# Kernel tuning notes

Measured on AMD Instinct MI355X. Metric: run time of the kernel, lower is better.

Reference implementation:

```python
import jax, jax.numpy as jnp
import numpy as np

B, S, D = 2, 2048, 2048
H, H_KV, HD = 8, 1, 256   # attention heads, kv heads, head_dim
N_REP = H // H_KV


def setup_inputs() -> dict:
    key = jax.random.key(0)
    ks = jax.random.split(key, 8)
    std = 1.0 / np.sqrt(D)
    return {
        "hidden_states": jax.random.normal(ks[0], (B, S, D), dtype=jnp.float32),
        "attention_mask": jnp.zeros((B, 1, S, S), dtype=jnp.float32),
        "cos": jax.random.uniform(ks[1], (B, S, HD), dtype=jnp.float32),
        "sin": jax.random.uniform(ks[2], (B, S, HD), dtype=jnp.float32),
        "Wq": jax.random.normal(ks[3], (D, H * HD), dtype=jnp.float32) * std,
        "Wk": jax.random.normal(ks[4], (D, H_KV * HD), dtype=jnp.float32) * std,
        "Wv": jax.random.normal(ks[5], (D, H_KV * HD), dtype=jnp.float32) * std,
        "Wo": jax.random.normal(ks[6], (H * HD, D), dtype=jnp.float32) * std,
    }


def _rotate_half(x):
    x1, x2 = jnp.split(x, 2, axis=-1)
    return jnp.concatenate((-x2, x1), axis=-1)


def reference(hidden_states, attention_mask, cos, sin, Wq, Wk, Wv, Wo):
    b, s, _ = hidden_states.shape
    # projections -> [b, heads, s, hd]
    q = (hidden_states @ Wq).reshape(b, s, H, HD).transpose(0, 2, 1, 3)
    k = (hidden_states @ Wk).reshape(b, s, H_KV, HD).transpose(0, 2, 1, 3)
    v = (hidden_states @ Wv).reshape(b, s, H_KV, HD).transpose(0, 2, 1, 3)
    # RoPE (unsqueeze_dim=1)
    c = cos[:, None, :, :]
    sn = sin[:, None, :, :]
    q = q * c + _rotate_half(q) * sn
    k = k * c + _rotate_half(k) * sn
    # GQA: repeat kv heads
    k = jnp.repeat(k, N_REP, axis=1)
    v = jnp.repeat(v, N_REP, axis=1)
    # attention
    scores = jnp.einsum("bhqd,bhkd->bhqk", q, k) / jnp.sqrt(jnp.float32(HD))
    scores = scores + attention_mask[:, :, :, :k.shape[2]]
    attn_weights = jax.nn.softmax(scores.astype(jnp.float32), axis=-1).astype(q.dtype)
    # dropout p=0.0 -> identity
    out = jnp.einsum("bhqk,bhkd->bhqd", attn_weights, v)
    out = out.transpose(0, 2, 1, 3).reshape(b, s, H * HD)
    out = out @ Wo
    return out, attn_weights
```

## Files before the change

kernel.cpp:

```cpp
#include <hip/hip_runtime.h>
#include <hip/hip_bf16.h>

typedef float f32x4 __attribute__((ext_vector_type(4)));
typedef short short8 __attribute__((ext_vector_type(8)));
typedef unsigned int uint2v __attribute__((ext_vector_type(2)));

#define DI __device__ __forceinline__

DI unsigned short f2bf(float f) {
  unsigned int u = __float_as_uint(f);
  u += 0x7fffu + ((u >> 16) & 1u);
  return (unsigned short)(u >> 16);
}

DI float bf2f(unsigned short u) {
  union { unsigned int i; float f; } x;
  x.i = ((unsigned int)u) << 16;
  return x.f;
}

DI unsigned int packbf(float a, float b) {
  return (unsigned int)f2bf(a) | ((unsigned int)f2bf(b) << 16);
}

DI void gload16(const unsigned short* g, unsigned short* l) {
  __builtin_amdgcn_global_load_lds((const __attribute__((address_space(1))) void*)g,
                                   (__attribute__((address_space(3))) void*)l, 16, 0, 0);
}

__global__ void cvt_bf16_kernel(const float* __restrict__ src,
                                unsigned short* __restrict__ dst, long n) {
  long i = ((long)blockIdx.x * blockDim.x + threadIdx.x) * 8;
  if (i >= n) return;
  f32x4 a = __builtin_nontemporal_load((const f32x4*)(src + i));
  f32x4 b = __builtin_nontemporal_load((const f32x4*)(src + i + 4));
  short8 v;
  v[0] = f2bf(a[0]); v[1] = f2bf(a[1]); v[2] = f2bf(a[2]); v[3] = f2bf(a[3]);
  v[4] = f2bf(b[0]); v[5] = f2bf(b[1]); v[6] = f2bf(b[2]); v[7] = f2bf(b[3]);
  *(short8*)(dst + i) = v;
}

__global__ void transpose_cvt_kernel(const float* __restrict__ src,
                                     unsigned short* __restrict__ dst,
                                     int ldsrc, int lddst, long sBatch, long dBatch) {
  __shared__ float tile[32][33];
  const float* s = src + (long)blockIdx.z * sBatch;
  unsigned short* d = dst + (long)blockIdx.z * dBatch;
  int c0 = blockIdx.x * 32, r0 = blockIdx.y * 32;
  int tx = threadIdx.x, ty = threadIdx.y;
#pragma unroll
  for (int k = 0; k < 4; k++)
    tile[ty + 8 * k][tx] =
        __builtin_nontemporal_load(s + (long)(r0 + ty + 8 * k) * ldsrc + c0 + tx);
  __syncthreads();
#pragma unroll
  for (int k = 0; k < 4; k++)
    d[(long)(c0 + ty + 8 * k) * lddst + r0 + tx] = f2bf(tile[tx][ty + 8 * k]);
}

__global__ void transpose_v_kernel(const float* __restrict__ qkv,
                                   unsigned short* __restrict__ VtC) {
  __shared__ float tile[32][33];
  int b = blockIdx.z;
  int d0 = blockIdx.x * 32, s0 = blockIdx.y * 32;
  int tx = threadIdx.x, ty = threadIdx.y;
  const float* s = qkv + (long)b * 2048 * 2560 + 2304;
#pragma unroll
  for (int k = 0; k < 4; k++)
    tile[ty + 8 * k][tx] = s[(long)(s0 + ty + 8 * k) * 2560 + d0 + tx];
  __syncthreads();
  unsigned short* d = VtC + (long)b * 524288 + (long)(s0 >> 5) * 8192;
#pragma unroll
  for (int k = 0; k < 4; k++) {
    int dd = d0 + ty + 8 * k;
    d[dd * 32 + (tx ^ (((dd >> 1) & 3) << 3))] = f2bf(tile[tx][ty + 8 * k]);
  }
}

__global__ void rope_kernel(const float* __restrict__ qkv, const float* __restrict__ cs,
                            const float* __restrict__ sn, unsigned short* __restrict__ Qb,
                            unsigned short* __restrict__ Ksw) {
  int bs = blockIdx.x;
  int d = threadIdx.x;
  long ci = (long)bs * 256 + d;
  float cv = cs[ci], sv = sn[ci];
  int b = bs >> 11, s2 = bs & 2047;
  const float* row = qkv + (long)bs * 2560;
  int off = (d < 128) ? 128 : -128;
  float sgn = (d < 128) ? -1.f : 1.f;
#pragma unroll
  for (int hp = 0; hp < 9; hp++) {
    float x = row[hp * 256 + d];
    float o = sgn * row[hp * 256 + d + off];
    unsigned short v = f2bf(x * cv + o * sv);
    if (hp < 8) {
      Qb[((long)(b * 8 + hp) * 2048 + s2) * 256 + d] = v;
    } else {
      Ksw[(long)bs * 256 + (d ^ ((bs & 7) << 3))] = v;
    }
  }
}

template <bool AF32, bool CBF16, bool CNT>
__launch_bounds__(256)
__global__ void gemm_bt_kernel(const void* __restrict__ Av,
                               const unsigned short* __restrict__ Btg,
                               void* __restrict__ Cv,
                               int K, int lda, int ldb, int ldc,
                               int zShift, long aBatch, long bBatch, long cBatch, long cHead) {
  __shared__ unsigned short Asm_[128 * 32];
  __shared__ unsigned short Bsm_[128 * 32];
  int z = blockIdx.z;
  int zb = z >> zShift, zh = z - (zb << zShift);
  const unsigned short* Bt = Btg + (long)zb * bBatch;
  const unsigned short* A16 = (const unsigned short*)Av + (long)z * aBatch;
  const float* A32 = (const float*)Av + (long)z * aBatch;
  int nwg = gridDim.x * gridDim.y;
  int bid = blockIdx.y * gridDim.x + blockIdx.x;
  int qq = nwg >> 3;
  int swz = (bid & 7) * qq + (bid >> 3);
  int m0 = (swz / gridDim.x) * 128, n0 = (swz % gridDim.x) * 128;
  int tid = threadIdx.x, w = tid >> 6, lane = tid & 63, c = lane & 15, t = lane >> 4;
  int wm = w >> 1, wn = w & 1;
  f32x4 zero4 = {0.f, 0.f, 0.f, 0.f};
  f32x4 acc[4][4];
#pragma unroll
  for (int i = 0; i < 4; i++)
#pragma unroll
    for (int j = 0; j < 4; j++) acc[i][j] = zero4;

  for (int kt = 0; kt < K; kt += 32) {
    if constexpr (!AF32) {
#pragma unroll
      for (int jj = 0; jj < 2; jj++) {
        int slot = (w * 2 + jj) * 64 + lane;
        int r = slot >> 2, g = slot & 3;
        int gs = g ^ ((r >> 1) & 3);
        gload16(A16 + (long)(m0 + r) * lda + kt + gs * 8, Asm_ + slot * 8);
      }
    } else {
#pragma unroll
      for (int jj = 0; jj < 2; jj++) {
        int slot = jj * 256 + tid;
        int r = slot >> 2, g = slot & 3;
        int gs = g ^ ((r >> 1) & 3);
        const float* p = A32 + (long)(m0 + r) * lda + kt + gs * 8;
        float4 x = *(const float4*)p;
        float4 y = *(const float4*)(p + 4);
        short8 v;
        v[0] = f2bf(x.x); v[1] = f2bf(x.y); v[2] = f2bf(x.z); v[3] = f2bf(x.w);
        v[4] = f2bf(y.x); v[5] = f2bf(y.y); v[6] = f2bf(y.z); v[7] = f2bf(y.w);
        *(short8*)(Asm_ + slot * 8) = v;
      }
    }
#pragma unroll
    for (int jj = 0; jj < 2; jj++) {
      int slot = (w * 2 + jj) * 64 + lane;
      int r = slot >> 2, g = slot & 3;
      int gs = g ^ ((r >> 1) & 3);
      gload16(Bt + (long)(n0 + r) * ldb + kt + gs * 8, Bsm_ + slot * 8);
    }
    __syncthreads();
    short8 af[4], bfg[4];
#pragma unroll
    for (int mi = 0; mi < 4; mi++) {
      int r = wm * 64 + mi * 16 + c;
      af[mi] = *(const short8*)(Asm_ + r * 32 + ((t ^ ((r >> 1) & 3)) * 8));
    }
#pragma unroll
    for (int ni = 0; ni < 4; ni++) {
      int r = wn * 64 + ni * 16 + c;
      bfg[ni] = *(const short8*)(Bsm_ + r * 32 + ((t ^ ((r >> 1) & 3)) * 8));
    }
#pragma unroll
    for (int mi = 0; mi < 4; mi++)
#pragma unroll
      for (int ni = 0; ni < 4; ni++)
        acc[mi][ni] = __builtin_amdgcn_mfma_f32_16x16x32_bf16(af[mi], bfg[ni], acc[mi][ni], 0, 0, 0);
    __syncthreads();
  }
  long cOff = (long)zb * cBatch + zh * cHead;
#pragma unroll
  for (int mi = 0; mi < 4; mi++) {
#pragma unroll
    for (int j = 0; j < 4; j++) {
      int row = m0 + wm * 64 + mi * 16 + t * 4 + j;
#pragma unroll
      for (int ni = 0; ni < 4; ni++) {
        int col = n0 + wn * 64 + ni * 16 + c;
        float v = acc[mi][ni][j];
        long idx = cOff + (long)row * ldc + col;
        if constexpr (CBF16) {
          ((unsigned short*)Cv)[idx] = f2bf(v);
        } else if constexpr (CNT) {
          __builtin_nontemporal_store(v, (float*)Cv + idx);
        } else {
          ((float*)Cv)[idx] = v;
        }
      }
    }
  }
}

#define KC 32
__launch_bounds__(512, 4)
__global__ void attn_fused_kernel(const unsigned short* __restrict__ Qb,
                                  const unsigned short* __restrict__ Ksw,
                                  const unsigned short* __restrict__ VtC,
                                  const float* __restrict__ mask,
                                  float* __restrict__ attnW,
                                  unsigned short* __restrict__ attnO) {
  __shared__ unsigned short Ksm[2][KC * 256];
  __shared__ unsigned short Vsm[2][256 * KC];
  __shared__ unsigned short Pt[2][4][16 * 32];
  __shared__ float red[8][16];
  const int id = blockIdx.x;
  const int sw = (id & 7) * 64 + (id >> 3);
  const int qblk = sw & 31, bh = sw >> 5;
  const int b = bh >> 3;
  const int tid = threadIdx.x, w = tid >> 6, lane = tid & 63;
  const int c = lane & 15, t = lane >> 4;
  const int s = w & 3, h = w >> 2;
  const int q0 = qblk * 64 + s * 16;
  const int kh = 16 * h;
  const float scale = 0.0625f;

  short8 qf[8];
  {
    const unsigned short* Qrow = Qb + ((long)bh * 2048 + q0 + c) * 256 + t * 8;
#pragma unroll
    for (int ks = 0; ks < 8; ks++) qf[ks] = *(const short8*)(Qrow + ks * 32);
  }

  const unsigned short* Kg = Ksw + (long)b * 524288;
  const unsigned short* Vg = VtC + (long)b * 524288;
  const float* mrow = mask + (long)b * 4194304 + (long)(q0 + c) * 2048 + kh + t * 4;

  float lp = 0.f;

#pragma unroll
  for (int i = 0; i < 2; i++) {
    int slot = i * 512 + tid;
    gload16(Kg + slot * 8, Ksm[0] + slot * 8);
  }
  f32x4 mv = *(const f32x4*)(mrow);
  for (int kc = 0; kc < 64; kc++) {
    int cur = kc & 1;
    asm volatile("s_barrier" ::: "memory");
    f32x4 mvn;
    if (kc < 63) {
      const unsigned short* src = Kg + (long)(kc + 1) * 8192;
#pragma unroll
      for (int i = 0; i < 2; i++) {
        int slot = i * 512 + tid;
        gload16(src + slot * 8, Ksm[cur ^ 1] + slot * 8);
      }
      mvn = *(const f32x4*)(mrow + (kc + 1) * 32);
      asm volatile("s_waitcnt vmcnt(3)" ::: "memory");
    } else {
      asm volatile("s_waitcnt vmcnt(0)" ::: "memory");
    }
    __builtin_amdgcn_sched_barrier(0);
    f32x4 a0 = {0.f, 0.f, 0.f, 0.f};
    __builtin_amdgcn_s_setprio(1);
#pragma unroll
    for (int ks = 0; ks < 8; ks++) {
      int g0 = ((ks * 4 + t) ^ (c & 7)) * 8;
      short8 kf = *(const short8*)(Ksm[cur] + (kh + c) * 256 + g0);
      a0 = __builtin_amdgcn_mfma_f32_16x16x32_bf16(kf, qf[ks], a0, 0, 0, 0);
    }
    __builtin_amdgcn_s_setprio(0);
#pragma unroll
    for (int j = 0; j < 4; j++) lp += __expf(a0[j] * scale + mv[j]);
    mv = mvn;
  }
  lp += __shfl_xor(lp, 16);
  lp += __shfl_xor(lp, 32);
  if (t == 0) red[w][c] = lp;
  __syncthreads();
  float rinv = 1.0f / (red[s][c] + red[4 + s][c]);

  float* awB = attnW + (long)bh * 4194304 + (long)(qblk * 64) * 2048;
  const int psw = ((c >> 1) & 3) << 3;
  const int srow = tid >> 3, sqk = tid & 7;
  const int ss2 = srow >> 4, sc2 = srow & 15;
  const int spsw = ((sc2 >> 1) & 3) << 3;
  const unsigned short* pRd = &Pt[0][ss2][0] + sc2 * 32 + ((sqk * 4) ^ spsw);
  const int ptStride = 4 * 16 * 32;
  float* awRow = awB + (long)srow * 2048 + sqk * 4;
  f32x4 accO[8];
#pragma unroll
  for (int i = 0; i < 8; i++) accO[i] = (f32x4){0.f, 0.f, 0.f, 0.f};

#pragma unroll
  for (int i = 0; i < 2; i++) {
    int slot = i * 512 + tid;
    gload16(Kg + slot * 8, Ksm[0] + slot * 8);
  }
  mv = *(const f32x4*)(mrow);
  for (int kc = 0; kc < 64; kc++) {
    int cur = kc & 1;
    asm volatile("s_barrier" ::: "memory");
    f32x4 mvn;
    if (kc < 63) {
      const unsigned short* ksrc = Kg + (long)(kc + 1) * 8192;
      const unsigned short* vsrc = Vg + (long)kc * 8192;
#pragma unroll
      for (int i = 0; i < 2; i++) {
        int slot = i * 512 + tid;
        gload16(ksrc + slot * 8, Ksm[cur ^ 1] + slot * 8);
        gload16(vsrc + slot * 8, Vsm[cur] + slot * 8);
      }
      mvn = *(const f32x4*)(mrow + (kc + 1) * 32);
      asm volatile("s_waitcnt vmcnt(5)" ::: "memory");
    } else {
      const unsigned short* vsrc = Vg + (long)kc * 8192;
#pragma unroll
      for (int i = 0; i < 2; i++) {
        int slot = i * 512 + tid;
        gload16(vsrc + slot * 8, Vsm[cur] + slot * 8);
      }
      asm volatile("s_waitcnt vmcnt(2)" ::: "memory");
    }
    __builtin_amdgcn_sched_barrier(0);
    f32x4 a0 = {0.f, 0.f, 0.f, 0.f};
    __builtin_amdgcn_s_setprio(1);
#pragma unroll
    for (int ks = 0; ks < 8; ks++) {
      int g0 = ((ks * 4 + t) ^ (c & 7)) * 8;
      short8 kf = *(const short8*)(Ksm[cur] + (kh + c) * 256 + g0);
      a0 = __builtin_amdgcn_mfma_f32_16x16x32_bf16(kf, qf[ks], a0, 0, 0, 0);
    }
    __builtin_amdgcn_s_setprio(0);
    f32x4 p;
#pragma unroll
    for (int j = 0; j < 4; j++) p[j] = __expf(a0[j] * scale + mv[j]) * rinv;
    mv = mvn;
    uint2v pw;
    pw[0] = packbf(p[0], p[1]); pw[1] = packbf(p[2], p[3]);
    *(uint2v*)(&Pt[cur][s][0] + c * 32 + ((kh + t * 4) ^ psw)) = pw;
    if (kc >= 1) {
      uint2v pu = *(const uint2v*)(pRd + (cur ^ 1) * ptStride);
      f32x4 aw;
      aw[0] = bf2f((unsigned short)(pu[0] & 0xffff));
      aw[1] = bf2f((unsigned short)(pu[0] >> 16));
      aw[2] = bf2f((unsigned short)(pu[1] & 0xffff));
      aw[3] = bf2f((unsigned short)(pu[1] >> 16));
      __builtin_nontemporal_store(aw, (f32x4*)(awRow + (kc - 1) * 32));
      short8 pa = *(const short8*)(&Pt[cur ^ 1][s][0] + c * 32 + ((t * 8) ^ psw));
      __builtin_amdgcn_s_setprio(1);
#pragma unroll
      for (int di = 0; di < 8; di++) {
        int d = (8 * h + di) * 16 + c;
        short8 vf = *(const short8*)(Vsm[cur ^ 1] + d * 32 + ((t * 8) ^ psw));
        accO[di] = __builtin_amdgcn_mfma_f32_16x16x32_bf16(pa, vf, accO[di], 0, 0, 0);
      }
      __builtin_amdgcn_s_setprio(0);
    }
    asm volatile("s_waitcnt lgkmcnt(0)" ::: "memory");
  }
  asm volatile("s_waitcnt vmcnt(0)" ::: "memory");
  __builtin_amdgcn_s_barrier();
  __builtin_amdgcn_sched_barrier(0);
  {
    uint2v pu = *(const uint2v*)(pRd + 1 * ptStride);
    f32x4 aw;
    aw[0] = bf2f((unsigned short)(pu[0] & 0xffff));
    aw[1] = bf2f((unsigned short)(pu[0] >> 16));
    aw[2] = bf2f((unsigned short)(pu[1] & 0xffff));
    aw[3] = bf2f((unsigned short)(pu[1] >> 16));
    __builtin_nontemporal_store(aw, (f32x4*)(awRow + 63 * 32));
    short8 pa = *(const short8*)(&Pt[1][s][0] + c * 32 + ((t * 8) ^ psw));
#pragma unroll
    for (int di = 0; di < 8; di++) {
      int d = (8 * h + di) * 16 + c;
      short8 vf = *(const short8*)(Vsm[1] + d * 32 + ((t * 8) ^ psw));
      accO[di] = __builtin_amdgcn_mfma_f32_16x16x32_bf16(pa, vf, accO[di], 0, 0, 0);
    }
  }
  long obase = ((long)b * 2048 + q0 + t * 4) * 2048 + (bh & 7) * 256 + h * 128 + c;
#pragma unroll
  for (int di = 0; di < 8; di++)
#pragma unroll
    for (int j = 0; j < 4; j++)
      __builtin_nontemporal_store(f2bf(accO[di][j]),
                                  attnO + obase + (long)j * 2048 + di * 16);
}

extern "C" void kernel_launch(void* const* d_in, const int* in_sizes, int n_in,
                              void* d_out, int out_size, void* d_ws, size_t ws_size,
                              hipStream_t stream) {
  const float* hidden = (const float*)d_in[0];
  const float* mask = (const float*)d_in[1];
  const float* cosb = (const float*)d_in[2];
  const float* sinb = (const float*)d_in[3];
  const float* Wq = (const float*)d_in[4];
  const float* Wk = (const float*)d_in[5];
  const float* Wv = (const float*)d_in[6];
  const float* Wo = (const float*)d_in[7];
  float* out = (float*)d_out;
  float* attnW = out + 8388608;

  char* ws = (char*)d_ws;
  unsigned short* hidB  = (unsigned short*)(ws + 0);
  unsigned short* WqkvT = (unsigned short*)(ws + 16777216);
  unsigned short* WoT   = (unsigned short*)(ws + 27262976);
  float*          qkv   = (float*)(ws + 35651584);
  unsigned short* Qb    = (unsigned short*)(ws + 77594624);
  unsigned short* Ksw   = (unsigned short*)(ws + 94371840);
  unsigned short* VtC   = (unsigned short*)(ws + 96468992);
  unsigned short* attnO = (unsigned short*)(ws + 98566144);

  cvt_bf16_kernel<<<4096, 256, 0, stream>>>(hidden, hidB, 8388608L);
  transpose_cvt_kernel<<<dim3(64, 64, 1), dim3(32, 8), 0, stream>>>(Wq, WqkvT, 2048, 2048, 0, 0);
  transpose_cvt_kernel<<<dim3(8, 64, 1), dim3(32, 8), 0, stream>>>(Wk, WqkvT + (long)2048 * 2048, 256, 2048, 0, 0);
  transpose_cvt_kernel<<<dim3(8, 64, 1), dim3(32, 8), 0, stream>>>(Wv, WqkvT + (long)2304 * 2048, 256, 2048, 0, 0);
  transpose_cvt_kernel<<<dim3(64, 64, 1), dim3(32, 8), 0, stream>>>(Wo, WoT, 2048, 2048, 0, 0);
  gemm_bt_kernel<false, false, false><<<dim3(20, 32, 1), 256, 0, stream>>>(
      hidB, WqkvT, qkv, 2048, 2048, 2048, 2560, 0, 0, 0, 0, 0);
  rope_kernel<<<4096, 256, 0, stream>>>(qkv, cosb, sinb, Qb, Ksw);
  transpose_v_kernel<<<dim3(8, 64, 2), dim3(32, 8), 0, stream>>>(qkv, VtC);
  attn_fused_kernel<<<512, 512, 0, stream>>>(Qb, Ksw, VtC, mask, attnW, attnO);
  gemm_bt_kernel<false, false, true><<<dim3(16, 32, 1), 256, 0, stream>>>(
      attnO, WoT, out, 2048, 2048, 2048, 2048, 0, 0, 0, 0, 0);
}
```

Measured before the change: 348.7 us.

## Halve attention block to four waves, each computing two 16-row query tiles

The fused attention kernel now runs 256 threads per block instead of 512. Each wave processes two 16-row query sub-tiles against each K/V fragment it loads from shared memory, so every LDS fragment read feeds two MFMAs. The change is meant to cut LDS read traffic and barrier cost per unit of work. In exchange, register pressure roughly doubles (two Q fragment sets, 16 output accumulators), the launch bounds drop to 2 blocks per CU, and each thread issues more global loads per chunk.

```diff
diff --git a/kernel.cpp b/kernel.cpp
--- a/kernel.cpp
+++ b/kernel.cpp
@@ -203,7 +203,7 @@
 }
 
 #define KC 32
-__launch_bounds__(512, 4)
+__launch_bounds__(256, 2)
 __global__ void attn_fused_kernel(const unsigned short* __restrict__ Qb,
                                   const unsigned short* __restrict__ Ksw,
                                   const unsigned short* __restrict__ VtC,
@@ -212,179 +212,220 @@
                                   unsigned short* __restrict__ attnO) {
   __shared__ unsigned short Ksm[2][KC * 256];
   __shared__ unsigned short Vsm[2][256 * KC];
-  __shared__ unsigned short Pt[2][4][16 * 32];
-  __shared__ float red[8][16];
+  __shared__ unsigned short Pt[2][2][2][16 * 32];
+  __shared__ float red[4][32];
   const int id = blockIdx.x;
   const int sw = (id & 7) * 64 + (id >> 3);
   const int qblk = sw & 31, bh = sw >> 5;
   const int b = bh >> 3;
   const int tid = threadIdx.x, w = tid >> 6, lane = tid & 63;
   const int c = lane & 15, t = lane >> 4;
-  const int s = w & 3, h = w >> 2;
-  const int q0 = qblk * 64 + s * 16;
+  const int g = w & 1, h = w >> 1;
+  const int qa = qblk * 64 + g * 32;
   const int kh = 16 * h;
   const float scale = 0.0625f;
 
-  short8 qf[8];
+  short8 qfa[8], qfb[8];
   {
-    const unsigned short* Qrow = Qb + ((long)bh * 2048 + q0 + c) * 256 + t * 8;
-#pragma unroll
-    for (int ks = 0; ks < 8; ks++) qf[ks] = *(const short8*)(Qrow + ks * 32);
+    const unsigned short* Qra = Qb + ((long)bh * 2048 + qa + c) * 256 + t * 8;
+    const unsigned short* Qrb = Qra + 16 * 256;
+#pragma unroll
+    for (int ks = 0; ks < 8; ks++) {
+      qfa[ks] = *(const short8*)(Qra + ks * 32);
+      qfb[ks] = *(const short8*)(Qrb + ks * 32);
+    }
   }
 
   const unsigned short* Kg = Ksw + (long)b * 524288;
   const unsigned short* Vg = VtC + (long)b * 524288;
-  const float* mrow = mask + (long)b * 4194304 + (long)(q0 + c) * 2048 + kh + t * 4;
-
-  float lp = 0.f;
-
-#pragma unroll
-  for (int i = 0; i < 2; i++) {
-    int slot = i * 512 + tid;
+  const float* mra = mask + (long)b * 4194304 + (long)(qa + c) * 2048 + kh + t * 4;
+  const float* mrb = mra + 16 * 2048;
+
+  float lp0 = 0.f, lp1 = 0.f;
+
+#pragma unroll
+  for (int i = 0; i < 4; i++) {
+    int slot = i * 256 + tid;
     gload16(Kg + slot * 8, Ksm[0] + slot * 8);
   }
-  f32x4 mv = *(const f32x4*)(mrow);
+  f32x4 mva = *(const f32x4*)(mra);
+  f32x4 mvb = *(const f32x4*)(mrb);
   for (int kc = 0; kc < 64; kc++) {
     int cur = kc & 1;
     asm volatile("s_barrier" ::: "memory");
-    f32x4 mvn;
+    f32x4 mna, mnb;
     if (kc < 63) {
       const unsigned short* src = Kg + (long)(kc + 1) * 8192;
 #pragma unroll
-      for (int i = 0; i < 2; i++) {
-        int slot = i * 512 + tid;
+      for (int i = 0; i < 4; i++) {
+        int slot = i * 256 + tid;
         gload16(src + slot * 8, Ksm[cur ^ 1] + slot * 8);
       }
-      mvn = *(const f32x4*)(mrow + (kc + 1) * 32);
-      asm volatile("s_waitcnt vmcnt(3)" ::: "memory");
+      mna = *(const f32x4*)(mra + (kc + 1) * 32);
+      mnb = *(const f32x4*)(mrb + (kc + 1) * 32);
+      asm volatile("s_waitcnt vmcnt(6)" ::: "memory");
     } else {
       asm volatile("s_waitcnt vmcnt(0)" ::: "memory");
     }
     __builtin_amdgcn_sched_barrier(0);
-    f32x4 a0 = {0.f, 0.f, 0.f, 0.f};
+    f32x4 a0 = {0.f, 0.f, 0.f, 0.f}, a1 = a0;
     __builtin_amdgcn_s_setprio(1);
 #pragma unroll
     for (int ks = 0; ks < 8; ks++) {
       int g0 = ((ks * 4 + t) ^ (c & 7)) * 8;
       short8 kf = *(const short8*)(Ksm[cur] + (kh + c) * 256 + g0);
-      a0 = __builtin_amdgcn_mfma_f32_16x16x32_bf16(kf, qf[ks], a0, 0, 0, 0);
+      a0 = __builtin_amdgcn_mfma_f32_16x16x32_bf16(kf, qfa[ks], a0, 0, 0, 0);
+      a1 = __builtin_amdgcn_mfma_f32_16x16x32_bf16(kf, qfb[ks], a1, 0, 0, 0);
     }
     __builtin_amdgcn_s_setprio(0);
 #pragma unroll
-    for (int j = 0; j < 4; j++) lp += __expf(a0[j] * scale + mv[j]);
-    mv = mvn;
-  }
-  lp += __shfl_xor(lp, 16);
-  lp += __shfl_xor(lp, 32);
-  if (t == 0) red[w][c] = lp;
+    for (int j = 0; j < 4; j++) {
+      lp0 += __expf(a0[j] * scale + mva[j]);
+      lp1 += __expf(a1[j] * scale + mvb[j]);
+    }
+    mva = mna; mvb = mnb;
+  }
+  lp0 += __shfl_xor(lp0, 16); lp0 += __shfl_xor(lp0, 32);
+  lp1 += __shfl_xor(lp1, 16); lp1 += __shfl_xor(lp1, 32);
+  if (t == 0) { red[w][c] = lp0; red[w][16 + c] = lp1; }
   __syncthreads();
-  float rinv = 1.0f / (red[s][c] + red[4 + s][c]);
-
+  float ri0 = 1.0f / (red[g][c] + red[g + 2][c]);
+  float ri1 = 1.0f / (red[g][16 + c] + red[g + 2][16 + c]);
+
+  const int psw = ((c >> 1) & 3) << 3;
   float* awB = attnW + (long)bh * 4194304 + (long)(qblk * 64) * 2048;
-  const int psw = ((c >> 1) & 3) << 3;
-  const int srow = tid >> 3, sqk = tid & 7;
-  const int ss2 = srow >> 4, sc2 = srow & 15;
-  const int spsw = ((sc2 >> 1) & 3) << 3;
-  const unsigned short* pRd = &Pt[0][ss2][0] + sc2 * 32 + ((sqk * 4) ^ spsw);
-  const int ptStride = 4 * 16 * 32;
-  float* awRow = awB + (long)srow * 2048 + sqk * 4;
-  f32x4 accO[8];
-#pragma unroll
-  for (int i = 0; i < 8; i++) accO[i] = (f32x4){0.f, 0.f, 0.f, 0.f};
-
-#pragma unroll
-  for (int i = 0; i < 2; i++) {
-    int slot = i * 512 + tid;
+  f32x4 accO[2][8];
+#pragma unroll
+  for (int i = 0; i < 2; i++)
+#pragma unroll
+    for (int j = 0; j < 8; j++) accO[i][j] = (f32x4){0.f, 0.f, 0.f, 0.f};
+
+#pragma unroll
+  for (int i = 0; i < 4; i++) {
+    int slot = i * 256 + tid;
     gload16(Kg + slot * 8, Ksm[0] + slot * 8);
   }
-  mv = *(const f32x4*)(mrow);
+  mva = *(const f32x4*)(mra);
+  mvb = *(const f32x4*)(mrb);
   for (int kc = 0; kc < 64; kc++) {
     int cur = kc & 1;
     asm volatile("s_barrier" ::: "memory");
-    f32x4 mvn;
+    f32x4 mna, mnb;
     if (kc < 63) {
       const unsigned short* ksrc = Kg + (long)(kc + 1) * 8192;
       const unsigned short* vsrc = Vg + (long)kc * 8192;
 #pragma unroll
-      for (int i = 0; i < 2; i++) {
-        int slot = i * 512 + tid;
+      for (int i = 0; i < 4; i++) {
+        int slot = i * 256 + tid;
         gload16(ksrc + slot * 8, Ksm[cur ^ 1] + slot * 8);
         gload16(vsrc + slot * 8, Vsm[cur] + slot * 8);
       }
-      mvn = *(const f32x4*)(mrow + (kc + 1) * 32);
-      asm volatile("s_waitcnt vmcnt(5)" ::: "memory");
+      mna = *(const f32x4*)(mra + (kc + 1) * 32);
+      mnb = *(const f32x4*)(mrb + (kc + 1) * 32);
+      asm volatile("s_waitcnt vmcnt(10)" ::: "memory");
     } else {
       const unsigned short* vsrc = Vg + (long)kc * 8192;
 #pragma unroll
-      for (int i = 0; i < 2; i++) {
-        int slot = i * 512 + tid;
+      for (int i = 0; i < 4; i++) {
+        int slot = i * 256 + tid;
         gload16(vsrc + slot * 8, Vsm[cur] + slot * 8);
       }
-      asm volatile("s_waitcnt vmcnt(2)" ::: "memory");
+      asm volatile("s_waitcnt vmcnt(4)" ::: "memory");
     }
     __builtin_amdgcn_sched_barrier(0);
-    f32x4 a0 = {0.f, 0.f, 0.f, 0.f};
+    f32x4 a0 = {0.f, 0.f, 0.f, 0.f}, a1 = a0;
     __builtin_amdgcn_s_setprio(1);
 #pragma unroll
     for (int ks = 0; ks < 8; ks++) {
       int g0 = ((ks * 4 + t) ^ (c & 7)) * 8;
       short8 kf = *(const short8*)(Ksm[cur] + (kh + c) * 256 + g0);
-      a0 = __builtin_amdgcn_mfma_f32_16x16x32_bf16(kf, qf[ks], a0, 0, 0, 0);
+      a0 = __builtin_amdgcn_mfma_f32_16x16x32_bf16(kf, qfa[ks], a0, 0, 0, 0);
+      a1 = __builtin_amdgcn_mfma_f32_16x16x32_bf16(kf, qfb[ks], a1, 0, 0, 0);
     }
     __builtin_amdgcn_s_setprio(0);
-    f32x4 p;
-#pragma unroll
-    for (int j = 0; j < 4; j++) p[j] = __expf(a0[j] * scale + mv[j]) * rinv;
-    mv = mvn;
-    uint2v pw;
-    pw[0] = packbf(p[0], p[1]); pw[1] = packbf(p[2], p[3]);
-    *(uint2v*)(&Pt[cur][s][0] + c * 32 + ((kh + t * 4) ^ psw)) = pw;
+    f32x4 p0, p1;
+#pragma unroll
+    for (int j = 0; j < 4; j++) {
+      p0[j] = __expf(a0[j] * scale + mva[j]) * ri0;
+      p1[j] = __expf(a1[j] * scale + mvb[j]) * ri1;
+    }
+    mva = mna; mvb = mnb;
+    uint2v pw0, pw1;
+    pw0[0] = packbf(p0[0], p0[1]); pw0[1] = packbf(p0[2], p0[3]);
+    pw1[0] = packbf(p1[0], p1[1]); pw1[1] = packbf(p1[2], p1[3]);
+    *(uint2v*)(&Pt[cur][g][0][0] + c * 32 + ((kh + t * 4) ^ psw)) = pw0;
+    *(uint2v*)(&Pt[cur][g][1][0] + c * 32 + ((kh + t * 4) ^ psw)) = pw1;
     if (kc >= 1) {
-      uint2v pu = *(const uint2v*)(pRd + (cur ^ 1) * ptStride);
+#pragma unroll
+      for (int li = 0; li < 2; li++) {
+        int slot2 = li * 256 + tid;
+        int srow = slot2 >> 3, sqk = slot2 & 7;
+        int sg = srow >> 5, ssub = (srow >> 4) & 1, sc2 = srow & 15;
+        int spsw2 = ((sc2 >> 1) & 3) << 3;
+        uint2v pu = *(const uint2v*)(&Pt[cur ^ 1][sg][ssub][0] + sc2 * 32 +
+                                     ((sqk * 4) ^ spsw2));
+        f32x4 aw;
+        aw[0] = bf2f((unsigned short)(pu[0] & 0xffff));
+        aw[1] = bf2f((unsigned short)(pu[0] >> 16));
+        aw[2] = bf2f((unsigned short)(pu[1] & 0xffff));
+        aw[3] = bf2f((unsigned short)(pu[1] >> 16));
+        __builtin_nontemporal_store(
+            aw, (f32x4*)(awB + (long)srow * 2048 + (kc - 1) * 32 + sqk * 4));
+      }
+      short8 pa0 = *(const short8*)(&Pt[cur ^ 1][g][0][0] + c * 32 + ((t * 8) ^ psw));
+      short8 pa1 = *(const short8*)(&Pt[cur ^ 1][g][1][0] + c * 32 + ((t * 8) ^ psw));
+      __builtin_amdgcn_s_setprio(1);
+#pragma unroll
+      for (int di = 0; di < 8; di++) {
+        int d = (8 * h + di) * 16 + c;
+        short8 vf = *(const short8*)(Vsm[cur ^ 1] + d * 32 + ((t * 8) ^ psw));
+        accO[0][di] = __builtin_amdgcn_mfma_f32_16x16x32_bf16(pa0, vf, accO[0][di], 0, 0, 0);
+        accO[1][di] = __builtin_amdgcn_mfma_f32_16x16x32_bf16(pa1, vf, accO[1][di], 0, 0, 0);
+      }
+      __builtin_amdgcn_s_setprio(0);
+    }
+    asm volatile("s_waitcnt lgkmcnt(0)" ::: "memory");
+  }
+  asm volatile("s_waitcnt vmcnt(0)" ::: "memory");
+  __builtin_amdgcn_s_barrier();
+  __builtin_amdgcn_sched_barrier(0);
+  {
+#pragma unroll
+    for (int li = 0; li < 2; li++) {
+      int slot2 = li * 256 + tid;
+      int srow = slot2 >> 3, sqk = slot2 & 7;
+      int sg = srow >> 5, ssub = (srow >> 4) & 1, sc2 = srow & 15;
+      int spsw2 = ((sc2 >> 1) & 3) << 3;
+      uint2v pu = *(const uint2v*)(&Pt[1][sg][ssub][0] + sc2 * 32 + ((sqk * 4) ^ spsw2));
       f32x4 aw;
       aw[0] = bf2f((unsigned short)(pu[0] & 0xffff));
       aw[1] = bf2f((unsigned short)(pu[0] >> 16));
       aw[2] = bf2f((unsigned short)(pu[1] & 0xffff));
       aw[3] = bf2f((unsigned short)(pu[1] >> 16));
-      __builtin_nontemporal_store(aw, (f32x4*)(awRow + (kc - 1) * 32));
-      short8 pa = *(const short8*)(&Pt[cur ^ 1][s][0] + c * 32 + ((t * 8) ^ psw));
-      __builtin_amdgcn_s_setprio(1);
-#pragma unroll
-      for (int di = 0; di < 8; di++) {
-        int d = (8 * h + di) * 16 + c;
-        short8 vf = *(const short8*)(Vsm[cur ^ 1] + d * 32 + ((t * 8) ^ psw));
-        accO[di] = __builtin_amdgcn_mfma_f32_16x16x32_bf16(pa, vf, accO[di], 0, 0, 0);
-      }
-      __builtin_amdgcn_s_setprio(0);
-    }
-    asm volatile("s_waitcnt lgkmcnt(0)" ::: "memory");
-  }
-  asm volatile("s_waitcnt vmcnt(0)" ::: "memory");
-  __builtin_amdgcn_s_barrier();
-  __builtin_amdgcn_sched_barrier(0);
-  {
-    uint2v pu = *(const uint2v*)(pRd + 1 * ptStride);
-    f32x4 aw;
-    aw[0] = bf2f((unsigned short)(pu[0] & 0xffff));
-    aw[1] = bf2f((unsigned short)(pu[0] >> 16));
-    aw[2] = bf2f((unsigned short)(pu[1] & 0xffff));
-    aw[3] = bf2f((unsigned short)(pu[1] >> 16));
-    __builtin_nontemporal_store(aw, (f32x4*)(awRow + 63 * 32));
-    short8 pa = *(const short8*)(&Pt[1][s][0] + c * 32 + ((t * 8) ^ psw));
+      __builtin_nontemporal_store(
+          aw, (f32x4*)(awB + (long)srow * 2048 + 63 * 32 + sqk * 4));
+    }
+    short8 pa0 = *(const short8*)(&Pt[1][g][0][0] + c * 32 + ((t * 8) ^ psw));
+    short8 pa1 = *(const short8*)(&Pt[1][g][1][0] + c * 32 + ((t * 8) ^ psw));
 #pragma unroll
     for (int di = 0; di < 8; di++) {
       int d = (8 * h + di) * 16 + c;
       short8 vf = *(const short8*)(Vsm[1] + d * 32 + ((t * 8) ^ psw));
-      accO[di] = __builtin_amdgcn_mfma_f32_16x16x32_bf16(pa, vf, accO[di], 0, 0, 0);
-    }
-  }
-  long obase = ((long)b * 2048 + q0 + t * 4) * 2048 + (bh & 7) * 256 + h * 128 + c;
+      accO[0][di] = __builtin_amdgcn_mfma_f32_16x16x32_bf16(pa0, vf, accO[0][di], 0, 0, 0);
+      accO[1][di] = __builtin_amdgcn_mfma_f32_16x16x32_bf16(pa1, vf, accO[1][di], 0, 0, 0);
+    }
+  }
+  long ob0 = ((long)b * 2048 + qa + t * 4) * 2048 + (bh & 7) * 256 + h * 128 + c;
+  long ob1 = ob0 + 16 * 2048;
 #pragma unroll
   for (int di = 0; di < 8; di++)
 #pragma unroll
-    for (int j = 0; j < 4; j++)
-      __builtin_nontemporal_store(f2bf(accO[di][j]),
-                                  attnO + obase + (long)j * 2048 + di * 16);
+    for (int j = 0; j < 4; j++) {
+      __builtin_nontemporal_store(f2bf(accO[0][di][j]),
+                                  attnO + ob0 + (long)j * 2048 + di * 16);
+      __builtin_nontemporal_store(f2bf(accO[1][di][j]),
+                                  attnO + ob1 + (long)j * 2048 + di * 16);
+    }
 }
 
 extern "C" void kernel_launch(void* const* d_in, const int* in_sizes, int n_in,
@@ -420,7 +461,7 @@
       hidB, WqkvT, qkv, 2048, 2048, 2048, 2560, 0, 0, 0, 0, 0);
   rope_kernel<<<4096, 256, 0, stream>>>(qkv, cosb, sinb, Qb, Ksw);
   transpose_v_kernel<<<dim3(8, 64, 2), dim3(32, 8), 0, stream>>>(qkv, VtC);
-  attn_fused_kernel<<<512, 512, 0, stream>>>(Qb, Ksw, VtC, mask, attnW, attnO);
+  attn_fused_kernel<<<512, 256, 0, stream>>>(Qb, Ksw, VtC, mask, attnW, attnO);
   gemm_bt_kernel<false, false, true><<<dim3(16, 32, 1), 256, 0, stream>>>(
       attnO, WoT, out, 2048, 2048, 2048, 2048, 0, 0, 0, 0, 0);
 }
```

Measured after the change: 352.0 us. About the same (+0.9%).
